# Performance work log

Hardware: AMD Instinct MI355X
Metric: run time of the kernel (lower is better)

## Reference

```python
import jax, jax.numpy as jnp
import numpy as np

B, L, V, H = 2, 2048, 1024, 16
HD = V // H  # head size 64
EPS = 1e-3   # keras LayerNormalization default


def setup_inputs() -> dict:
    key = jax.random.key(0)
    ks = jax.random.split(key, 10)
    scale = 1.0 / np.sqrt(V)
    return {
        "query": jax.random.normal(ks[0], (B, L, V), jnp.float32),
        "key_t": jax.random.normal(ks[1], (B, L, V), jnp.float32),
        "value": jax.random.normal(ks[2], (B, L, V), jnp.float32),
        "Wq": jax.random.normal(ks[3], (H, V, HD), jnp.float32) * scale,
        "Wk": jax.random.normal(ks[4], (H, V, HD), jnp.float32) * scale,
        "Wv": jax.random.normal(ks[5], (H, V, HD), jnp.float32) * scale,
        "gamma": jnp.ones((V,), jnp.float32),
        "beta": jnp.zeros((V,), jnp.float32),
        "query_mask": jax.random.randint(ks[6], (B, L), 0, 2, jnp.int32),
        "value_mask": jax.random.randint(ks[7], (B, L), 0, 2, jnp.int32),
    }


def reference(query, key_t, value, Wq, Wk, Wv, gamma, beta, query_mask, value_mask):
    qm = query_mask.astype(jnp.float32)  # (B,L)
    vm = value_mask.astype(jnp.float32)  # (B,L)

    # per-head no-bias Dense projections, batched over heads
    Q = jnp.einsum('blv,hvd->bhld', query, Wq)
    K = jnp.einsum('blv,hvd->bhld', key_t, Wk)
    Vh = jnp.einsum('blv,hvd->bhld', value, Wv)

    scores = jnp.einsum('bhld,bhmd->bhlm', Q, K) / jnp.sqrt(jnp.float32(HD))
    attn = jax.nn.softmax(scores, axis=-1)

    # post-softmax multiplicative masking (faithful to original)
    tri = jnp.tril(jnp.ones((L, L), jnp.float32))  # (L,L) causal
    attn = attn * tri[None, None, :, :]
    attn = attn * qm[:, None, :, None] * vm[:, None, None, :]

    heads = jnp.einsum('bhlm,bhmd->bhld', attn, Vh)
    x = heads.transpose(0, 2, 1, 3).reshape(B, L, V)  # concat heads

    # dropout is identity at inference
    y = x + query
    mu = jnp.mean(y, axis=-1, keepdims=True)
    var = jnp.mean((y - mu) ** 2, axis=-1, keepdims=True)
    return gamma * (y - mu) * jax.lax.rsqrt(var + EPS) + beta
```

## Files before the change

### kernel.cpp

```cpp
#include <hip/hip_runtime.h>
#include <math.h>

constexpr int NB = 2;
constexpr int SL = 2048;
constexpr int NV = 1024;
constexpr int NH = 16;
constexpr int DH = 64;
constexpr int NT = SL / 64;
constexpr float LN_EPS = 1e-3f;

typedef __bf16 bf16_t;
typedef __bf16 v8bf __attribute__((ext_vector_type(8)));
typedef float  v4f  __attribute__((ext_vector_type(4)));

__device__ __forceinline__ v8bf cvt8(float4 a, float4 b) {
  v8bf v;
  v[0] = (bf16_t)a.x; v[1] = (bf16_t)a.y; v[2] = (bf16_t)a.z; v[3] = (bf16_t)a.w;
  v[4] = (bf16_t)b.x; v[5] = (bf16_t)b.y; v[6] = (bf16_t)b.z; v[7] = (bf16_t)b.w;
  return v;
}
__device__ __forceinline__ unsigned pack_bf16(float a, float b) {
  unsigned short ua = __builtin_bit_cast(unsigned short, (bf16_t)a);
  unsigned short ub = __builtin_bit_cast(unsigned short, (bf16_t)b);
  return (unsigned)ua | ((unsigned)ub << 16);
}
__device__ __forceinline__ void async_cp16(const void* g, void* l) {
  __builtin_amdgcn_global_load_lds(
      (const __attribute__((address_space(1))) unsigned int*)g,
      (__attribute__((address_space(3))) unsigned int*)l, 16, 0, 0);
}

__global__ __launch_bounds__(256)
void wcvt(const float* __restrict__ Wq, const float* __restrict__ Wk,
          const float* __restrict__ Wv, bf16_t* __restrict__ Wt) {
  __shared__ float ls[64][65];
  const int z = blockIdx.z;
  const float* W = z == 0 ? Wq : (z == 1 ? Wk : Wv);
  const float sc = z == 0 ? 0.125f * 1.44269504f : 1.0f;
  const int h = blockIdx.y, v0 = blockIdx.x * 64;
  const int t = threadIdx.x;
  const int rr = t >> 4, c4 = t & 15;
  const float* src = W + ((size_t)h * NV + v0) * DH;
#pragma unroll
  for (int it = 0; it < 4; ++it) {
    float4 f = *(const float4*)(src + (size_t)(rr + it * 16) * DH + c4 * 4);
    ls[rr + it * 16][c4 * 4 + 0] = f.x;
    ls[rr + it * 16][c4 * 4 + 1] = f.y;
    ls[rr + it * 16][c4 * 4 + 2] = f.z;
    ls[rr + it * 16][c4 * 4 + 3] = f.w;
  }
  __syncthreads();
  const int dd = t >> 2, vq = t & 3;
  bf16_t tmp[16];
#pragma unroll
  for (int i = 0; i < 16; ++i) tmp[i] = (bf16_t)(ls[vq * 16 + i][dd] * sc);
  bf16_t* dst = Wt + ((size_t)z * NV + h * 64 + dd) * NV + v0 + vq * 16;
  *(v8bf*)dst = *(v8bf*)&tmp[0];
  *(v8bf*)(dst + 8) = *(v8bf*)&tmp[8];
}

__global__ __launch_bounds__(256, 3)
void proj_mfma(const float* __restrict__ A0, const float* __restrict__ A1,
               const float* __restrict__ A2, const bf16_t* __restrict__ Wtb,
               bf16_t* __restrict__ O0, bf16_t* __restrict__ O1,
               bf16_t* __restrict__ O2) {
  __shared__ __align__(16) float  As[128 * 64];
  __shared__ __align__(16) bf16_t Wsh[128 * 64];

  const int z = blockIdx.z;
  const float*  A   = z == 0 ? A0 : (z == 1 ? A1 : A2);
  bf16_t*       out = z == 0 ? O0 : (z == 1 ? O1 : O2);
  const bf16_t* W   = Wtb + (size_t)z * NV * NV;

  const int t = threadIdx.x, w = t >> 6, lane = t & 63;
  const int g = lane >> 4, lx = lane & 15;
  const int m0 = blockIdx.x * 128, n0 = blockIdx.y * 128;
  const int rbase = (w >> 1) * 64, cbase = (w & 1) * 64;

  const int ra_off = lane >> 4;
  const int ca_l   = lane & 15;
  const int rw_off = lane >> 3;
  const int cw_l   = lane & 7;

  v4f acc[4][4] = {};

  for (int k0 = 0; k0 < NV; k0 += 64) {
    __syncthreads();
#pragma unroll
    for (int s = 0; s < 8; ++s) {
      const int ra  = w * 32 + s * 4 + ra_off;
      const int cga = ca_l ^ (ra & 7);
      async_cp16(A + (size_t)(m0 + ra) * NV + k0 + cga * 4,
                 (char*)As + (w * 32 + s * 4) * 256);
    }
#pragma unroll
    for (int s = 0; s < 4; ++s) {
      const int rw  = w * 32 + s * 8 + rw_off;
      const int cgw = cw_l ^ (rw_off & 7);
      async_cp16(W + (size_t)(n0 + rw) * NV + k0 + cgw * 8,
                 (char*)Wsh + (w * 32 + s * 8) * 128);
    }
    __syncthreads();
#pragma unroll
    for (int ks = 0; ks < 2; ++ks) {
      v8bf af[4], bfr[4];
#pragma unroll
      for (int rt = 0; rt < 4; ++rt) {
        const int row = rbase + rt * 16 + lx;
        const int sw = lx & 7;
        const int c0 = ks * 8 + g * 2;
        float4 f0 = *(const float4*)((const char*)As + row * 256 + ((c0    ) ^ sw) * 16);
        float4 f1 = *(const float4*)((const char*)As + row * 256 + ((c0 + 1) ^ sw) * 16);
        af[rt] = cvt8(f0, f1);
      }
#pragma unroll
      for (int ct = 0; ct < 4; ++ct) {
        const int row = cbase + ct * 16 + lx;
        const int c = ks * 4 + g;
        bfr[ct] = *(const v8bf*)((const char*)Wsh + row * 128 + (c ^ (lx & 7)) * 16);
      }
#pragma unroll
      for (int rt = 0; rt < 4; ++rt)
#pragma unroll
        for (int ct = 0; ct < 4; ++ct)
          acc[rt][ct] = __builtin_amdgcn_mfma_f32_16x16x32_bf16(
              af[rt], bfr[ct], acc[rt][ct], 0, 0, 0);
    }
  }

#pragma unroll
  for (int rt = 0; rt < 4; ++rt) {
#pragma unroll
    for (int reg = 0; reg < 4; ++reg) {
      const int row = m0 + rbase + rt * 16 + g * 4 + reg;
      const int b = row >> 11, l = row & (SL - 1);
#pragma unroll
      for (int ct = 0; ct < 4; ++ct) {
        const int n = n0 + cbase + ct * 16 + lx;
        const int h = n >> 6, d = n & 63;
        out[((size_t)(b * NH + h) * SL + l) * DH + d] = (bf16_t)acc[rt][ct][reg];
      }
    }
  }
}

__global__ __launch_bounds__(256, 3)
void attn_mfma(const bf16_t* __restrict__ Qg, const bf16_t* __restrict__ Kg,
               const bf16_t* __restrict__ Vg, const int* __restrict__ qmask,
               const int* __restrict__ vmask, float* __restrict__ Xout) {
  __shared__ __align__(16) bf16_t kbuf[2][64 * 64];
  __shared__ bf16_t Vt[2][64][72];
  __shared__ bf16_t Ps[4][16][72];

  const int id = blockIdx.x;
  const int bh = (id & 7) | ((id >> 8) << 3);
  const int qb = (id >> 3) & 31;
  const int t = threadIdx.x, w = t >> 6, lane = t & 63;
  const int g = lane >> 4, lx = lane & 15;
  const int b = bh >> 4, h = bh & 15;
  const int l0 = qb * 64;

  const bf16_t* Kb = Kg + (size_t)bh * SL * DH;
  const bf16_t* Vb = Vg + (size_t)bh * SL * DH;

  const bf16_t* Qrow = Qg + ((size_t)bh * SL + l0 + w * 16 + lx) * DH;
  v8bf qf0 = *(const v8bf*)(Qrow + g * 8);
  v8bf qf1 = *(const v8bf*)(Qrow + 32 + g * 8);

  v4f O[4] = {};
  float suml = 0.f;

  const int vtp = t & 31, vtd = t >> 5, vmb = b * SL;

  const int kr_off = lane >> 3;
  const int ks_l   = lane & 7;
  auto stageK = [&](int mb, int buf) {
#pragma unroll
    for (int s = 0; s < 2; ++s) {
      const int r = w * 16 + s * 8 + kr_off;
      const int c = ks_l ^ (r & 7);
      async_cp16(Kb + (size_t)(mb + r) * DH + c * 8,
                 (char*)kbuf[buf] + (w * 16 + s * 8) * 128);
    }
  };
  auto readK = [&](int buf, int ks, int ct) -> v8bf {
    const int rr = ct * 16 + lx;
    const int slot = (ks * 4 + g) ^ (lx & 7);
    return *(const v8bf*)((const char*)kbuf[buf] + rr * 128 + slot * 16);
  };

  uint4 vr0, vr1;
  unsigned vmsk0, vmsk1;
  auto loadV = [&](int mb) {
    const bf16_t* vsrc = Vb + (size_t)(mb + 2 * vtp) * DH + vtd * 8;
    vmsk0 = vmask[vmb + mb + 2 * vtp]     ? 0xffffffffu : 0u;
    vmsk1 = vmask[vmb + mb + 2 * vtp + 1] ? 0xffffffffu : 0u;
    vr0 = *(const uint4*)vsrc;
    vr1 = *(const uint4*)(vsrc + DH);
  };

  stageK(0, 0);
  loadV(0);

  for (int mt = 0; mt <= qb; ++mt) {
    const int m0 = mt * 64, pb = mt & 1;
    {
      const unsigned w0[4] = {vr0.x & vmsk0, vr0.y & vmsk0, vr0.z & vmsk0, vr0.w & vmsk0};
      const unsigned w1[4] = {vr1.x & vmsk1, vr1.y & vmsk1, vr1.z & vmsk1, vr1.w & vmsk1};
#pragma unroll
      for (int i = 0; i < 4; ++i) {
        unsigned lo = (w0[i] & 0xffffu) | (w1[i] << 16);
        unsigned hi = (w0[i] >> 16) | (w1[i] & 0xffff0000u);
        *(unsigned*)&Vt[pb][vtd * 8 + 2 * i][2 * vtp]     = lo;
        *(unsigned*)&Vt[pb][vtd * 8 + 2 * i + 1][2 * vtp] = hi;
      }
    }
    __syncthreads();
    if (mt + 1 < NT) stageK(m0 + 64, pb ^ 1);
    if (mt < qb) loadV(m0 + 64);

    v4f S[4] = {};
#pragma unroll
    for (int ks = 0; ks < 2; ++ks) {
      const v8bf qf = ks ? qf1 : qf0;
#pragma unroll
      for (int ct = 0; ct < 4; ++ct)
        S[ct] = __builtin_amdgcn_mfma_f32_16x16x32_bf16(readK(pb, ks, ct), qf,
                                                        S[ct], 0, 0, 0);
    }

    const bool diag = (mt == qb);
    if (!diag) {
#pragma unroll
      for (int ct = 0; ct < 4; ++ct) {
        float e0 = __builtin_amdgcn_exp2f(S[ct][0]);
        float e1 = __builtin_amdgcn_exp2f(S[ct][1]);
        float e2 = __builtin_amdgcn_exp2f(S[ct][2]);
        float e3 = __builtin_amdgcn_exp2f(S[ct][3]);
        suml += (e0 + e1) + (e2 + e3);
        uint2 u = {pack_bf16(e0, e1), pack_bf16(e2, e3)};
        *(uint2*)&Ps[w][lx][ct * 16 + g * 4] = u;
      }
    } else {
      const int l_loc = w * 16 + lx;
#pragma unroll
      for (int ct = 0; ct < 4; ++ct) {
        float e0 = __builtin_amdgcn_exp2f(S[ct][0]);
        float e1 = __builtin_amdgcn_exp2f(S[ct][1]);
        float e2 = __builtin_amdgcn_exp2f(S[ct][2]);
        float e3 = __builtin_amdgcn_exp2f(S[ct][3]);
        suml += (e0 + e1) + (e2 + e3);
        const int mb = ct * 16 + g * 4;
        float p0 = (mb + 0 <= l_loc) ? e0 : 0.f;
        float p1 = (mb + 1 <= l_loc) ? e1 : 0.f;
        float p2 = (mb + 2 <= l_loc) ? e2 : 0.f;
        float p3 = (mb + 3 <= l_loc) ? e3 : 0.f;
        uint2 u = {pack_bf16(p0, p1), pack_bf16(p2, p3)};
        *(uint2*)&Ps[w][lx][ct * 16 + g * 4] = u;
      }
    }

#pragma unroll
    for (int ks = 0; ks < 2; ++ks) {
      v8bf pf = *(const v8bf*)&Ps[w][lx][ks * 32 + g * 8];
#pragma unroll
      for (int dt = 0; dt < 4; ++dt) {
        v8bf vf = *(const v8bf*)&Vt[pb][dt * 16 + lx][ks * 32 + g * 8];
        O[dt] = __builtin_amdgcn_mfma_f32_16x16x32_bf16(pf, vf, O[dt], 0, 0, 0);
      }
    }
  }

  for (int mt = qb + 1; mt < NT; ++mt) {
    const int pb = mt & 1;
    __syncthreads();
    if (mt + 1 < NT) stageK(mt * 64 + 64, pb ^ 1);
    v4f S[4] = {};
#pragma unroll
    for (int ks = 0; ks < 2; ++ks) {
      const v8bf qf = ks ? qf1 : qf0;
#pragma unroll
      for (int ct = 0; ct < 4; ++ct)
        S[ct] = __builtin_amdgcn_mfma_f32_16x16x32_bf16(readK(pb, ks, ct), qf,
                                                        S[ct], 0, 0, 0);
    }
#pragma unroll
    for (int ct = 0; ct < 4; ++ct)
#pragma unroll
      for (int r = 0; r < 4; ++r)
        suml += __builtin_amdgcn_exp2f(S[ct][r]);
  }

  suml += __shfl_xor(suml, 16);
  suml += __shfl_xor(suml, 32);

#pragma unroll
  for (int reg = 0; reg < 4; ++reg) {
    const int lg = l0 + w * 16 + g * 4 + reg;
    const float den = __shfl(suml, g * 4 + reg);
    const float inv = (float)qmask[b * SL + lg] / den;
#pragma unroll
    for (int dt = 0; dt < 4; ++dt)
      Xout[((size_t)(b * SL + lg)) * NV + h * DH + dt * 16 + lx] =
          O[dt][reg] * inv;
  }
}

__global__ __launch_bounds__(256)
void ln_kernel(const float* __restrict__ X, const float* __restrict__ query,
               const float* __restrict__ gamma, const float* __restrict__ beta,
               float* __restrict__ out) {
  const int row = blockIdx.x;
  const int t = threadIdx.x;
  const float* xr = X + (size_t)row * NV;
  const float* qr = query + (size_t)row * NV;
  float4 xv = *(const float4*)(xr + t * 4);
  float4 qv = *(const float4*)(qr + t * 4);
  float y[4] = {xv.x + qv.x, xv.y + qv.y, xv.z + qv.z, xv.w + qv.w};
  float s  = y[0] + y[1] + y[2] + y[3];
  float ss = y[0]*y[0] + y[1]*y[1] + y[2]*y[2] + y[3]*y[3];
#pragma unroll
  for (int off = 1; off < 64; off <<= 1) {
    s  += __shfl_xor(s, off);
    ss += __shfl_xor(ss, off);
  }
  __shared__ float ws_s[4], ws_ss[4];
  const int wid = t >> 6;
  if ((t & 63) == 0) { ws_s[wid] = s; ws_ss[wid] = ss; }
  __syncthreads();
  s  = ws_s[0] + ws_s[1] + ws_s[2] + ws_s[3];
  ss = ws_ss[0] + ws_ss[1] + ws_ss[2] + ws_ss[3];
  const float mu   = s * (1.f / NV);
  const float var  = ss * (1.f / NV) - mu * mu;
  const float rstd = rsqrtf(var + LN_EPS);
  float4 gv = *(const float4*)(gamma + t * 4);
  float4 bv = *(const float4*)(beta + t * 4);
  float4 o;
  o.x = gv.x * (y[0] - mu) * rstd + bv.x;
  o.y = gv.y * (y[1] - mu) * rstd + bv.y;
  o.z = gv.z * (y[2] - mu) * rstd + bv.z;
  o.w = gv.w * (y[3] - mu) * rstd + bv.w;
  *(float4*)(out + (size_t)row * NV + t * 4) = o;
}

extern "C" void kernel_launch(void* const* d_in, const int* in_sizes, int n_in,
                              void* d_out, int out_size, void* d_ws, size_t ws_size,
                              hipStream_t stream) {
  const float* query = (const float*)d_in[0];
  const float* key_t = (const float*)d_in[1];
  const float* value = (const float*)d_in[2];
  const float* Wq    = (const float*)d_in[3];
  const float* Wk    = (const float*)d_in[4];
  const float* Wv    = (const float*)d_in[5];
  const float* gamma = (const float*)d_in[6];
  const float* beta  = (const float*)d_in[7];
  const int*   qmask = (const int*)d_in[8];
  const int*   vmask = (const int*)d_in[9];
  float* out = (float*)d_out;

  const size_t per = (size_t)NB * NH * SL * DH;
  bf16_t* Qws = (bf16_t*)d_ws;
  bf16_t* Kws = Qws + per;
  bf16_t* Vws = Kws + per;
  bf16_t* Wtb = Vws + per;

  wcvt<<<dim3(16, 16, 3), 256, 0, stream>>>(Wq, Wk, Wv, Wtb);
  proj_mfma<<<dim3(32, 8, 3), 256, 0, stream>>>(query, key_t, value, Wtb,
                                                Qws, Kws, Vws);
  attn_mfma<<<1024, 256, 0, stream>>>(Qws, Kws, Vws, qmask, vmask, out);
  ln_kernel<<<NB * SL, 256, 0, stream>>>(out, query, gamma, beta, out);
}
```

Before: 232.2 us.

## Double-buffer projection, pre-transpose masked V, split attention key range across waves

```diff
diff --git a/kernel.cpp b/kernel.cpp
--- a/kernel.cpp
+++ b/kernel.cpp
@@ -62,10 +62,11 @@
 __global__ __launch_bounds__(256, 3)
 void proj_mfma(const float* __restrict__ A0, const float* __restrict__ A1,
                const float* __restrict__ A2, const bf16_t* __restrict__ Wtb,
+               const int* __restrict__ vmask,
                bf16_t* __restrict__ O0, bf16_t* __restrict__ O1,
                bf16_t* __restrict__ O2) {
-  __shared__ __align__(16) float  As[128 * 64];
-  __shared__ __align__(16) bf16_t Wsh[128 * 64];
+  __shared__ __align__(16) float  As[2][128 * 32];
+  __shared__ __align__(16) bf16_t Wsh[2][128 * 32];
 
   const int z = blockIdx.z;
   const float*  A   = z == 0 ? A0 : (z == 1 ? A1 : A2);
@@ -77,68 +78,86 @@
   const int m0 = blockIdx.x * 128, n0 = blockIdx.y * 128;
   const int rbase = (w >> 1) * 64, cbase = (w & 1) * 64;
 
-  const int ra_off = lane >> 4;
-  const int ca_l   = lane & 15;
-  const int rw_off = lane >> 3;
-  const int cw_l   = lane & 7;
+  auto stageA = [&](int k0, int buf) {
+#pragma unroll
+    for (int s = 0; s < 4; ++s) {
+      const int r = w * 32 + s * 8 + (lane >> 3);
+      const int c = (lane & 7) ^ (r & 7);
+      async_cp16(A + (size_t)(m0 + r) * NV + k0 + c * 4,
+                 (char*)As[buf] + (w * 32 + s * 8) * 128);
+    }
+  };
+  auto stageW = [&](int k0, int buf) {
+#pragma unroll
+    for (int s = 0; s < 2; ++s) {
+      const int r = w * 32 + s * 16 + (lane >> 2);
+      const int c = (lane & 3) ^ (r & 3);
+      async_cp16(W + (size_t)(n0 + r) * NV + k0 + c * 8,
+                 (char*)Wsh[buf] + (w * 32 + s * 16) * 64);
+    }
+  };
 
   v4f acc[4][4] = {};
-
-  for (int k0 = 0; k0 < NV; k0 += 64) {
+  stageA(0, 0);
+  stageW(0, 0);
+
+  for (int k0 = 0; k0 < NV; k0 += 32) {
+    const int buf = (k0 >> 5) & 1;
     __syncthreads();
-#pragma unroll
-    for (int s = 0; s < 8; ++s) {
-      const int ra  = w * 32 + s * 4 + ra_off;
-      const int cga = ca_l ^ (ra & 7);
-      async_cp16(A + (size_t)(m0 + ra) * NV + k0 + cga * 4,
-                 (char*)As + (w * 32 + s * 4) * 256);
-    }
-#pragma unroll
-    for (int s = 0; s < 4; ++s) {
-      const int rw  = w * 32 + s * 8 + rw_off;
-      const int cgw = cw_l ^ (rw_off & 7);
-      async_cp16(W + (size_t)(n0 + rw) * NV + k0 + cgw * 8,
-                 (char*)Wsh + (w * 32 + s * 8) * 128);
-    }
-    __syncthreads();
-#pragma unroll
-    for (int ks = 0; ks < 2; ++ks) {
-      v8bf af[4], bfr[4];
-#pragma unroll
-      for (int rt = 0; rt < 4; ++rt) {
-        const int row = rbase + rt * 16 + lx;
-        const int sw = lx & 7;
-        const int c0 = ks * 8 + g * 2;
-        float4 f0 = *(const float4*)((const char*)As + row * 256 + ((c0    ) ^ sw) * 16);
-        float4 f1 = *(const float4*)((const char*)As + row * 256 + ((c0 + 1) ^ sw) * 16);
-        af[rt] = cvt8(f0, f1);
-      }
-#pragma unroll
-      for (int ct = 0; ct < 4; ++ct) {
-        const int row = cbase + ct * 16 + lx;
-        const int c = ks * 4 + g;
-        bfr[ct] = *(const v8bf*)((const char*)Wsh + row * 128 + (c ^ (lx & 7)) * 16);
-      }
-#pragma unroll
-      for (int rt = 0; rt < 4; ++rt)
-#pragma unroll
-        for (int ct = 0; ct < 4; ++ct)
-          acc[rt][ct] = __builtin_amdgcn_mfma_f32_16x16x32_bf16(
-              af[rt], bfr[ct], acc[rt][ct], 0, 0, 0);
-    }
-  }
-
-#pragma unroll
-  for (int rt = 0; rt < 4; ++rt) {
-#pragma unroll
-    for (int reg = 0; reg < 4; ++reg) {
-      const int row = m0 + rbase + rt * 16 + g * 4 + reg;
+    if (k0 + 32 < NV) { stageA(k0 + 32, buf ^ 1); stageW(k0 + 32, buf ^ 1); }
+    v8bf af[4], wf[4];
+#pragma unroll
+    for (int rt = 0; rt < 4; ++rt) {
+      const int row = rbase + rt * 16 + lx;
+      const int sw = row & 7;
+      float4 f0 = *(const float4*)((const char*)As[buf] + row * 128 + ((2 * g)     ^ sw) * 16);
+      float4 f1 = *(const float4*)((const char*)As[buf] + row * 128 + ((2 * g + 1) ^ sw) * 16);
+      af[rt] = cvt8(f0, f1);
+    }
+#pragma unroll
+    for (int ct = 0; ct < 4; ++ct) {
+      const int row = cbase + ct * 16 + lx;
+      wf[ct] = *(const v8bf*)((const char*)Wsh[buf] + row * 64 + (g ^ (row & 3)) * 16);
+    }
+#pragma unroll
+    for (int rt = 0; rt < 4; ++rt)
+#pragma unroll
+      for (int ct = 0; ct < 4; ++ct)
+        acc[rt][ct] = __builtin_amdgcn_mfma_f32_16x16x32_bf16(
+            af[rt], wf[ct], acc[rt][ct], 0, 0, 0);
+  }
+
+  if (z < 2) {
+#pragma unroll
+    for (int rt = 0; rt < 4; ++rt) {
+#pragma unroll
+      for (int reg = 0; reg < 4; ++reg) {
+        const int row = m0 + rbase + rt * 16 + g * 4 + reg;
+        const int b = row >> 11, l = row & (SL - 1);
+#pragma unroll
+        for (int ct = 0; ct < 4; ++ct) {
+          const int n = n0 + cbase + ct * 16 + lx;
+          const int h = n >> 6, d = n & 63;
+          out[((size_t)(b * NH + h) * SL + l) * DH + d] = (bf16_t)acc[rt][ct][reg];
+        }
+      }
+    }
+  } else {
+#pragma unroll
+    for (int rt = 0; rt < 4; ++rt) {
+      const int row = m0 + rbase + rt * 16 + g * 4;
       const int b = row >> 11, l = row & (SL - 1);
+      float vm0 = (float)vmask[b * SL + l + 0];
+      float vm1 = (float)vmask[b * SL + l + 1];
+      float vm2 = (float)vmask[b * SL + l + 2];
+      float vm3 = (float)vmask[b * SL + l + 3];
 #pragma unroll
       for (int ct = 0; ct < 4; ++ct) {
         const int n = n0 + cbase + ct * 16 + lx;
         const int h = n >> 6, d = n & 63;
-        out[((size_t)(b * NH + h) * SL + l) * DH + d] = (bf16_t)acc[rt][ct][reg];
+        uint2 u = {pack_bf16(acc[rt][ct][0] * vm0, acc[rt][ct][1] * vm1),
+                   pack_bf16(acc[rt][ct][2] * vm2, acc[rt][ct][3] * vm3)};
+        *(uint2*)&out[((size_t)(b * NH + h) * DH + d) * SL + l] = u;
       }
     }
   }
@@ -146,128 +165,114 @@
 
 __global__ __launch_bounds__(256, 3)
 void attn_mfma(const bf16_t* __restrict__ Qg, const bf16_t* __restrict__ Kg,
-               const bf16_t* __restrict__ Vg, const int* __restrict__ qmask,
-               const int* __restrict__ vmask, float* __restrict__ Xout) {
-  __shared__ __align__(16) bf16_t kbuf[2][64 * 64];
-  __shared__ bf16_t Vt[2][64][72];
-  __shared__ bf16_t Ps[4][16][72];
+               const bf16_t* __restrict__ Vtg_all, const int* __restrict__ qmask,
+               float* __restrict__ Xout) {
+  struct LoopBufs { bf16_t kbuf[2][64 * 64]; bf16_t vbuf[2][64 * 64]; };
+  union __align__(16) SU { LoopBufs lp; float Obuf[2][64][36]; };
+  __shared__ SU su;
+  __shared__ bf16_t Ps[64][72];
+  __shared__ float sums[2][64];
 
   const int id = blockIdx.x;
   const int bh = (id & 7) | ((id >> 8) << 3);
-  const int qb = (id >> 3) & 31;
+  const int qb = 31 - ((id >> 3) & 31);
   const int t = threadIdx.x, w = t >> 6, lane = t & 63;
   const int g = lane >> 4, lx = lane & 15;
+  const int mh = w >> 1, qh = w & 1;
   const int b = bh >> 4, h = bh & 15;
   const int l0 = qb * 64;
 
-  const bf16_t* Kb = Kg + (size_t)bh * SL * DH;
-  const bf16_t* Vb = Vg + (size_t)bh * SL * DH;
-
-  const bf16_t* Qrow = Qg + ((size_t)bh * SL + l0 + w * 16 + lx) * DH;
-  v8bf qf0 = *(const v8bf*)(Qrow + g * 8);
-  v8bf qf1 = *(const v8bf*)(Qrow + 32 + g * 8);
-
-  v4f O[4] = {};
-  float suml = 0.f;
-
-  const int vtp = t & 31, vtd = t >> 5, vmb = b * SL;
-
-  const int kr_off = lane >> 3;
-  const int ks_l   = lane & 7;
+  const bf16_t* Kb  = Kg + (size_t)bh * SL * DH;
+  const bf16_t* Vtg = Vtg_all + (size_t)bh * DH * SL;
+
+  v8bf qf[2][2];
+#pragma unroll
+  for (int qt = 0; qt < 2; ++qt)
+#pragma unroll
+    for (int ks = 0; ks < 2; ++ks)
+      qf[qt][ks] = *(const v8bf*)&Qg[((size_t)bh * SL + l0 + qh * 32 + qt * 16 + lx) * DH +
+                                     ks * 32 + g * 8];
+
+  v4f O[2][4] = {};
+  float suml[2] = {0.f, 0.f};
+
   auto stageK = [&](int mb, int buf) {
 #pragma unroll
     for (int s = 0; s < 2; ++s) {
-      const int r = w * 16 + s * 8 + kr_off;
-      const int c = ks_l ^ (r & 7);
+      const int r = w * 16 + s * 8 + (lane >> 3);
+      const int c = (lane & 7) ^ (r & 7);
       async_cp16(Kb + (size_t)(mb + r) * DH + c * 8,
-                 (char*)kbuf[buf] + (w * 16 + s * 8) * 128);
+                 (char*)su.lp.kbuf[buf] + (w * 16 + s * 8) * 128);
     }
   };
-  auto readK = [&](int buf, int ks, int ct) -> v8bf {
-    const int rr = ct * 16 + lx;
-    const int slot = (ks * 4 + g) ^ (lx & 7);
-    return *(const v8bf*)((const char*)kbuf[buf] + rr * 128 + slot * 16);
+  auto stageV = [&](int mb, int buf) {
+#pragma unroll
+    for (int s = 0; s < 2; ++s) {
+      const int r = w * 16 + s * 8 + (lane >> 3);
+      const int c = (lane & 7) ^ (r & 7);
+      async_cp16(Vtg + (size_t)r * SL + mb + c * 8,
+                 (char*)su.lp.vbuf[buf] + (w * 16 + s * 8) * 128);
+    }
   };
 
-  uint4 vr0, vr1;
-  unsigned vmsk0, vmsk1;
-  auto loadV = [&](int mb) {
-    const bf16_t* vsrc = Vb + (size_t)(mb + 2 * vtp) * DH + vtd * 8;
-    vmsk0 = vmask[vmb + mb + 2 * vtp]     ? 0xffffffffu : 0u;
-    vmsk1 = vmask[vmb + mb + 2 * vtp + 1] ? 0xffffffffu : 0u;
-    vr0 = *(const uint4*)vsrc;
-    vr1 = *(const uint4*)(vsrc + DH);
-  };
-
   stageK(0, 0);
-  loadV(0);
+  stageV(0, 0);
 
   for (int mt = 0; mt <= qb; ++mt) {
     const int m0 = mt * 64, pb = mt & 1;
-    {
-      const unsigned w0[4] = {vr0.x & vmsk0, vr0.y & vmsk0, vr0.z & vmsk0, vr0.w & vmsk0};
-      const unsigned w1[4] = {vr1.x & vmsk1, vr1.y & vmsk1, vr1.z & vmsk1, vr1.w & vmsk1};
-#pragma unroll
-      for (int i = 0; i < 4; ++i) {
-        unsigned lo = (w0[i] & 0xffffu) | (w1[i] << 16);
-        unsigned hi = (w0[i] >> 16) | (w1[i] & 0xffff0000u);
-        *(unsigned*)&Vt[pb][vtd * 8 + 2 * i][2 * vtp]     = lo;
-        *(unsigned*)&Vt[pb][vtd * 8 + 2 * i + 1][2 * vtp] = hi;
-      }
-    }
     __syncthreads();
-    if (mt + 1 < NT) stageK(m0 + 64, pb ^ 1);
-    if (mt < qb) loadV(m0 + 64);
-
-    v4f S[4] = {};
-#pragma unroll
-    for (int ks = 0; ks < 2; ++ks) {
-      const v8bf qf = ks ? qf1 : qf0;
-#pragma unroll
-      for (int ct = 0; ct < 4; ++ct)
-        S[ct] = __builtin_amdgcn_mfma_f32_16x16x32_bf16(readK(pb, ks, ct), qf,
-                                                        S[ct], 0, 0, 0);
-    }
+    if (mt + 1 < NT)  stageK(m0 + 64, pb ^ 1);
+    if (mt + 1 <= qb) stageV(m0 + 64, pb ^ 1);
+
+    v4f S[2][2] = {};
+#pragma unroll
+    for (int ks = 0; ks < 2; ++ks)
+#pragma unroll
+      for (int mt2 = 0; mt2 < 2; ++mt2) {
+        const int row = mh * 32 + mt2 * 16 + lx;
+        const int slot = (ks * 4 + g) ^ (row & 7);
+        v8bf kf = *(const v8bf*)((const char*)su.lp.kbuf[pb] + row * 128 + slot * 16);
+#pragma unroll
+        for (int qt = 0; qt < 2; ++qt)
+          S[mt2][qt] = __builtin_amdgcn_mfma_f32_16x16x32_bf16(
+              kf, qf[qt][ks], S[mt2][qt], 0, 0, 0);
+      }
 
     const bool diag = (mt == qb);
-    if (!diag) {
-#pragma unroll
-      for (int ct = 0; ct < 4; ++ct) {
-        float e0 = __builtin_amdgcn_exp2f(S[ct][0]);
-        float e1 = __builtin_amdgcn_exp2f(S[ct][1]);
-        float e2 = __builtin_amdgcn_exp2f(S[ct][2]);
-        float e3 = __builtin_amdgcn_exp2f(S[ct][3]);
-        suml += (e0 + e1) + (e2 + e3);
+#pragma unroll
+    for (int mt2 = 0; mt2 < 2; ++mt2)
+#pragma unroll
+      for (int qt = 0; qt < 2; ++qt) {
+        float e0 = __builtin_amdgcn_exp2f(S[mt2][qt][0]);
+        float e1 = __builtin_amdgcn_exp2f(S[mt2][qt][1]);
+        float e2 = __builtin_amdgcn_exp2f(S[mt2][qt][2]);
+        float e3 = __builtin_amdgcn_exp2f(S[mt2][qt][3]);
+        suml[qt] += (e0 + e1) + (e2 + e3);
+        if (diag) {
+          const int ml = mh * 32 + mt2 * 16 + g * 4;
+          const int ql = qh * 32 + qt * 16 + lx;
+          e0 = (ml + 0 <= ql) ? e0 : 0.f;
+          e1 = (ml + 1 <= ql) ? e1 : 0.f;
+          e2 = (ml + 2 <= ql) ? e2 : 0.f;
+          e3 = (ml + 3 <= ql) ? e3 : 0.f;
+        }
         uint2 u = {pack_bf16(e0, e1), pack_bf16(e2, e3)};
-        *(uint2*)&Ps[w][lx][ct * 16 + g * 4] = u;
-      }
-    } else {
-      const int l_loc = w * 16 + lx;
-#pragma unroll
-      for (int ct = 0; ct < 4; ++ct) {
-        float e0 = __builtin_amdgcn_exp2f(S[ct][0]);
-        float e1 = __builtin_amdgcn_exp2f(S[ct][1]);
-        float e2 = __builtin_amdgcn_exp2f(S[ct][2]);
-        float e3 = __builtin_amdgcn_exp2f(S[ct][3]);
-        suml += (e0 + e1) + (e2 + e3);
-        const int mb = ct * 16 + g * 4;
-        float p0 = (mb + 0 <= l_loc) ? e0 : 0.f;
-        float p1 = (mb + 1 <= l_loc) ? e1 : 0.f;
-        float p2 = (mb + 2 <= l_loc) ? e2 : 0.f;
-        float p3 = (mb + 3 <= l_loc) ? e3 : 0.f;
-        uint2 u = {pack_bf16(p0, p1), pack_bf16(p2, p3)};
-        *(uint2*)&Ps[w][lx][ct * 16 + g * 4] = u;
-      }
-    }
-
-#pragma unroll
-    for (int ks = 0; ks < 2; ++ks) {
-      v8bf pf = *(const v8bf*)&Ps[w][lx][ks * 32 + g * 8];
-#pragma unroll
-      for (int dt = 0; dt < 4; ++dt) {
-        v8bf vf = *(const v8bf*)&Vt[pb][dt * 16 + lx][ks * 32 + g * 8];
-        O[dt] = __builtin_amdgcn_mfma_f32_16x16x32_bf16(pf, vf, O[dt], 0, 0, 0);
-      }
+        *(uint2*)&Ps[qh * 32 + qt * 16 + lx][mh * 32 + mt2 * 16 + g * 4] = u;
+      }
+
+    v8bf pf[2];
+#pragma unroll
+    for (int qt = 0; qt < 2; ++qt)
+      pf[qt] = *(const v8bf*)&Ps[qh * 32 + qt * 16 + lx][mh * 32 + g * 8];
+#pragma unroll
+    for (int dt = 0; dt < 4; ++dt) {
+      const int row = dt * 16 + lx;
+      const int slot = (mh * 4 + g) ^ (row & 7);
+      v8bf vf = *(const v8bf*)((const char*)su.lp.vbuf[pb] + row * 128 + slot * 16);
+#pragma unroll
+      for (int qt = 0; qt < 2; ++qt)
+        O[qt][dt] = __builtin_amdgcn_mfma_f32_16x16x32_bf16(
+            pf[qt], vf, O[qt][dt], 0, 0, 0);
     }
   }
 
@@ -275,34 +280,62 @@
     const int pb = mt & 1;
     __syncthreads();
     if (mt + 1 < NT) stageK(mt * 64 + 64, pb ^ 1);
-    v4f S[4] = {};
-#pragma unroll
-    for (int ks = 0; ks < 2; ++ks) {
-      const v8bf qf = ks ? qf1 : qf0;
-#pragma unroll
-      for (int ct = 0; ct < 4; ++ct)
-        S[ct] = __builtin_amdgcn_mfma_f32_16x16x32_bf16(readK(pb, ks, ct), qf,
-                                                        S[ct], 0, 0, 0);
-    }
-#pragma unroll
-    for (int ct = 0; ct < 4; ++ct)
-#pragma unroll
-      for (int r = 0; r < 4; ++r)
-        suml += __builtin_amdgcn_exp2f(S[ct][r]);
-  }
-
-  suml += __shfl_xor(suml, 16);
-  suml += __shfl_xor(suml, 32);
-
-#pragma unroll
-  for (int reg = 0; reg < 4; ++reg) {
-    const int lg = l0 + w * 16 + g * 4 + reg;
-    const float den = __shfl(suml, g * 4 + reg);
-    const float inv = (float)qmask[b * SL + lg] / den;
-#pragma unroll
-    for (int dt = 0; dt < 4; ++dt)
-      Xout[((size_t)(b * SL + lg)) * NV + h * DH + dt * 16 + lx] =
-          O[dt][reg] * inv;
+    v4f S[2][2] = {};
+#pragma unroll
+    for (int ks = 0; ks < 2; ++ks)
+#pragma unroll
+      for (int mt2 = 0; mt2 < 2; ++mt2) {
+        const int row = mh * 32 + mt2 * 16 + lx;
+        const int slot = (ks * 4 + g) ^ (row & 7);
+        v8bf kf = *(const v8bf*)((const char*)su.lp.kbuf[pb] + row * 128 + slot * 16);
+#pragma unroll
+        for (int qt = 0; qt < 2; ++qt)
+          S[mt2][qt] = __builtin_amdgcn_mfma_f32_16x16x32_bf16(
+              kf, qf[qt][ks], S[mt2][qt], 0, 0, 0);
+      }
+#pragma unroll
+    for (int mt2 = 0; mt2 < 2; ++mt2)
+#pragma unroll
+      for (int qt = 0; qt < 2; ++qt)
+        suml[qt] += (__builtin_amdgcn_exp2f(S[mt2][qt][0]) +
+                     __builtin_amdgcn_exp2f(S[mt2][qt][1])) +
+                    (__builtin_amdgcn_exp2f(S[mt2][qt][2]) +
+                     __builtin_amdgcn_exp2f(S[mt2][qt][3]));
+  }
+
+  suml[0] += __shfl_xor(suml[0], 16); suml[0] += __shfl_xor(suml[0], 32);
+  suml[1] += __shfl_xor(suml[1], 16); suml[1] += __shfl_xor(suml[1], 32);
+  __syncthreads();
+  if (g == 0) {
+    sums[mh][qh * 32 + lx]      = suml[0];
+    sums[mh][qh * 32 + 16 + lx] = suml[1];
+  }
+  if (mh == 0) {
+#pragma unroll
+    for (int qt = 0; qt < 2; ++qt)
+#pragma unroll
+      for (int dt = 0; dt < 4; ++dt)
+        *(v4f*)&su.Obuf[qh][dt * 16 + lx][qt * 16 + g * 4] = O[qt][dt];
+  }
+  __syncthreads();
+  if (mh == 1) {
+#pragma unroll
+    for (int qt = 0; qt < 2; ++qt) {
+#pragma unroll
+      for (int dt = 0; dt < 4; ++dt)
+        O[qt][dt] += *(const v4f*)&su.Obuf[qh][dt * 16 + lx][qt * 16 + g * 4];
+#pragma unroll
+      for (int reg = 0; reg < 4; ++reg) {
+        const int ql = qh * 32 + qt * 16 + g * 4 + reg;
+        const int q = l0 + ql;
+        const float den = sums[0][ql] + sums[1][ql];
+        const float inv = (float)qmask[b * SL + q] / den;
+#pragma unroll
+        for (int dt = 0; dt < 4; ++dt)
+          Xout[((size_t)(b * SL + q)) * NV + h * DH + dt * 16 + lx] =
+              O[qt][dt][reg] * inv;
+      }
+    }
   }
 }
 
@@ -310,37 +343,47 @@
 void ln_kernel(const float* __restrict__ X, const float* __restrict__ query,
                const float* __restrict__ gamma, const float* __restrict__ beta,
                float* __restrict__ out) {
-  const int row = blockIdx.x;
+  const int row0 = blockIdx.x * 2;
   const int t = threadIdx.x;
-  const float* xr = X + (size_t)row * NV;
-  const float* qr = query + (size_t)row * NV;
-  float4 xv = *(const float4*)(xr + t * 4);
-  float4 qv = *(const float4*)(qr + t * 4);
-  float y[4] = {xv.x + qv.x, xv.y + qv.y, xv.z + qv.z, xv.w + qv.w};
-  float s  = y[0] + y[1] + y[2] + y[3];
-  float ss = y[0]*y[0] + y[1]*y[1] + y[2]*y[2] + y[3]*y[3];
-#pragma unroll
-  for (int off = 1; off < 64; off <<= 1) {
-    s  += __shfl_xor(s, off);
-    ss += __shfl_xor(ss, off);
-  }
-  __shared__ float ws_s[4], ws_ss[4];
-  const int wid = t >> 6;
-  if ((t & 63) == 0) { ws_s[wid] = s; ws_ss[wid] = ss; }
-  __syncthreads();
-  s  = ws_s[0] + ws_s[1] + ws_s[2] + ws_s[3];
-  ss = ws_ss[0] + ws_ss[1] + ws_ss[2] + ws_ss[3];
-  const float mu   = s * (1.f / NV);
-  const float var  = ss * (1.f / NV) - mu * mu;
-  const float rstd = rsqrtf(var + LN_EPS);
   float4 gv = *(const float4*)(gamma + t * 4);
   float4 bv = *(const float4*)(beta + t * 4);
-  float4 o;
-  o.x = gv.x * (y[0] - mu) * rstd + bv.x;
-  o.y = gv.y * (y[1] - mu) * rstd + bv.y;
-  o.z = gv.z * (y[2] - mu) * rstd + bv.z;
-  o.w = gv.w * (y[3] - mu) * rstd + bv.w;
-  *(float4*)(out + (size_t)row * NV + t * 4) = o;
+  float y[2][4];
+  float s[2], ss[2];
+#pragma unroll
+  for (int r = 0; r < 2; ++r) {
+    float4 xv = *(const float4*)(X + (size_t)(row0 + r) * NV + t * 4);
+    float4 qv = *(const float4*)(query + (size_t)(row0 + r) * NV + t * 4);
+    y[r][0] = xv.x + qv.x; y[r][1] = xv.y + qv.y;
+    y[r][2] = xv.z + qv.z; y[r][3] = xv.w + qv.w;
+    s[r]  = (y[r][0] + y[r][1]) + (y[r][2] + y[r][3]);
+    ss[r] = (y[r][0]*y[r][0] + y[r][1]*y[r][1]) + (y[r][2]*y[r][2] + y[r][3]*y[r][3]);
+  }
+#pragma unroll
+  for (int off = 1; off < 64; off <<= 1) {
+    s[0]  += __shfl_xor(s[0], off);  ss[0] += __shfl_xor(ss[0], off);
+    s[1]  += __shfl_xor(s[1], off);  ss[1] += __shfl_xor(ss[1], off);
+  }
+  __shared__ float wsum[2][2][4];
+  const int wid = t >> 6;
+  if ((t & 63) == 0) {
+    wsum[0][0][wid] = s[0]; wsum[0][1][wid] = ss[0];
+    wsum[1][0][wid] = s[1]; wsum[1][1][wid] = ss[1];
+  }
+  __syncthreads();
+#pragma unroll
+  for (int r = 0; r < 2; ++r) {
+    float sr  = (wsum[r][0][0] + wsum[r][0][1]) + (wsum[r][0][2] + wsum[r][0][3]);
+    float ssr = (wsum[r][1][0] + wsum[r][1][1]) + (wsum[r][1][2] + wsum[r][1][3]);
+    const float mu   = sr * (1.f / NV);
+    const float var  = ssr * (1.f / NV) - mu * mu;
+    const float rstd = rsqrtf(var + LN_EPS);
+    float4 o;
+    o.x = gv.x * (y[r][0] - mu) * rstd + bv.x;
+    o.y = gv.y * (y[r][1] - mu) * rstd + bv.y;
+    o.z = gv.z * (y[r][2] - mu) * rstd + bv.z;
+    o.w = gv.w * (y[r][3] - mu) * rstd + bv.w;
+    *(float4*)(out + (size_t)(row0 + r) * NV + t * 4) = o;
+  }
 }
 
 extern "C" void kernel_launch(void* const* d_in, const int* in_sizes, int n_in,
@@ -366,7 +409,7 @@
 
   wcvt<<<dim3(16, 16, 3), 256, 0, stream>>>(Wq, Wk, Wv, Wtb);
   proj_mfma<<<dim3(32, 8, 3), 256, 0, stream>>>(query, key_t, value, Wtb,
-                                                Qws, Kws, Vws);
-  attn_mfma<<<1024, 256, 0, stream>>>(Qws, Kws, Vws, qmask, vmask, out);
-  ln_kernel<<<NB * SL, 256, 0, stream>>>(out, query, gamma, beta, out);
-}
+                                                vmask, Qws, Kws, Vws);
+  attn_mfma<<<1024, 256, 0, stream>>>(Qws, Kws, Vws, qmask, out);
+  ln_kernel<<<NB * SL / 2, 256, 0, stream>>>(out, query, gamma, beta, out);
+}
```

New measurement: 226.8 us. 1.02x faster.
